# Optimization experiments

Measured on AMD Instinct MI355X. Metric: run time of the kernel, lower is better.

## Reference

```python
import jax, jax.numpy as jnp
import numpy as np

B, C1, C2, D, NH, H, W = 2, 64, 256, 256, 8, 64, 64
HD = D // NH
EPS = 1e-5


def setup_inputs() -> dict:
    key = jax.random.key(0)
    ks = jax.random.split(key, 12)
    s = lambda fan_in: 1.0 / np.sqrt(fan_in)
    return {
        "F_lidar": jax.random.normal(ks[0], (B, C1, H, W), jnp.float32),
        "F_cam": jax.random.normal(ks[1], (B, C2, H, W), jnp.float32),
        "Wq": jax.random.normal(ks[2], (D, C1), jnp.float32) * s(C1),
        "Wk": jax.random.normal(ks[3], (D, C2), jnp.float32) * s(C2),
        "Wv": jax.random.normal(ks[4], (D, C2), jnp.float32) * s(C2),
        "Wo": jax.random.normal(ks[5], (D, D), jnp.float32) * s(D),
        "Wres": jax.random.normal(ks[6], (D, C1), jnp.float32) * s(C1),
        "g1": jnp.ones((D,), jnp.float32),
        "b1": jnp.zeros((D,), jnp.float32),
        "g2": jnp.ones((D,), jnp.float32),
        "b2": jnp.zeros((D,), jnp.float32),
        "W1": jax.random.normal(ks[7], (4 * D, D), jnp.float32) * s(D),
        "bf1": jnp.zeros((4 * D,), jnp.float32),
        "W2": jax.random.normal(ks[8], (D, 4 * D), jnp.float32) * s(4 * D),
        "bf2": jnp.zeros((D,), jnp.float32),
    }


def _layernorm(x, g, b):
    mu = jnp.mean(x, axis=-1, keepdims=True)
    var = jnp.mean(jnp.square(x - mu), axis=-1, keepdims=True)
    return (x - mu) * jax.lax.rsqrt(var + EPS) * g + b


def reference(F_lidar, F_cam, Wq, Wk, Wv, Wo, Wres, g1, b1, g2, b2, W1, bf1, W2, bf2):
    b, _, h, w = F_lidar.shape
    n = h * w
    # channels-last token views: (B, HW, C)
    xl = F_lidar.reshape(b, C1, n).transpose(0, 2, 1)
    xc = F_cam.reshape(b, C2, n).transpose(0, 2, 1)
    # 1x1 conv projections == per-token matmuls
    Q = jnp.einsum('bnc,dc->bnd', xl, Wq).reshape(b, n, NH, HD).transpose(0, 2, 1, 3)
    K = jnp.einsum('bnc,dc->bnd', xc, Wk).reshape(b, n, NH, HD).transpose(0, 2, 1, 3)
    V = jnp.einsum('bnc,dc->bnd', xc, Wv).reshape(b, n, NH, HD).transpose(0, 2, 1, 3)
    scale = HD ** -0.5
    scores = jnp.einsum('bhqd,bhkd->bhqk', Q, K) * scale  # (B,NH,HW,HW)
    attn = jax.nn.softmax(scores, axis=-1)
    out = jnp.einsum('bhqk,bhkd->bhqd', attn, V)
    out = out.transpose(0, 2, 1, 3).reshape(b, n, D)
    out = jnp.einsum('bnd,ed->bne', out, Wo)
    resid = jnp.einsum('bnc,dc->bnd', xl, Wres)
    x = _layernorm(resid + out, g1, b1)
    # FFN (dropout = identity in eval)
    hdn = jax.nn.relu(jnp.einsum('bnd,fd->bnf', x, W1) + bf1)
    ffn = jnp.einsum('bnf,df->bnd', hdn, W2) + bf2
    x = _layernorm(x + ffn, g2, b2)
    return x.transpose(0, 2, 1).reshape(b, D, h, w)
```

## Files before the change

### kernel.cpp

```cpp
#include <hip/hip_runtime.h>
#include <hip/hip_bf16.h>
#include <math.h>

#define NB 2
#define C1 64
#define C2 256
#define DD 256
#define NHH 8
#define HDD 32
#define NN 4096
#define FF 1024
#define MTOT (NB*NN)
#define KVB 128

typedef unsigned short u16;
typedef __attribute__((ext_vector_type(8))) short bf16x8;
typedef __attribute__((ext_vector_type(4))) float f32x4;
typedef __attribute__((ext_vector_type(4))) unsigned short us4;
typedef __attribute__((ext_vector_type(4))) unsigned int u32x4;

__device__ __forceinline__ u16 f2bf(float f) {
    union { float f; unsigned int i; } u; u.f = f;
    unsigned int r = u.i + 0x7FFFu + ((u.i >> 16) & 1u);
    return (u16)(r >> 16);
}

__device__ __forceinline__ unsigned cvt_pk_bf16(float a, float b) {
    unsigned r; asm("v_cvt_pk_bf16_f32 %0, %1, %2" : "=v"(r) : "v"(a), "v"(b)); return r;
}

__device__ __forceinline__ void glds16(const void* g, void* l) {
    __builtin_amdgcn_global_load_lds(
        (__attribute__((address_space(1))) void*)g,
        (__attribute__((address_space(3))) void*)l, 16, 0, 0);
}

__global__ __launch_bounds__(256) void wconv(
    const float* __restrict__ Wq, const float* __restrict__ Wres,
    const float* __restrict__ Wk, const float* __restrict__ Wv,
    const float* __restrict__ Wo, const float* __restrict__ W1,
    const float* __restrict__ W2, u16* __restrict__ d)
{
    int i = blockIdx.x * 256 + threadIdx.x;
    if (i >= 753664) return;
    const float* s; int off;
    if      (i <  16384) { s = Wq;   off = i; }
    else if (i <  32768) { s = Wres; off = i -  16384; }
    else if (i <  98304) { s = Wk;   off = i -  32768; }
    else if (i < 163840) { s = Wv;   off = i -  98304; }
    else if (i < 229376) { s = Wo;   off = i - 163840; }
    else if (i < 491520) { s = W1;   off = i - 229376; }
    else                 { s = W2;   off = i - 491520; }
    d[i] = f2bf(s[off]);
}

__global__ __launch_bounds__(256) void tconv(const float* __restrict__ src,
                                             u16* __restrict__ dst, int C)
{
    __shared__ float tile[64][65];
    const int n0 = blockIdx.x * 64;
    const int c0 = blockIdx.y * 64;
    const int b  = blockIdx.z;
    const int t  = threadIdx.x;
#pragma unroll
    for (int i = 0; i < 4; ++i) {
        int cc = t + i * 256;
        int c = cc >> 4, off = (cc & 15) * 4;
        const float4 v = *(const float4*)&src[((size_t)b*C + c0 + c)*NN + n0 + off];
        tile[c][off+0] = v.x; tile[c][off+1] = v.y;
        tile[c][off+2] = v.z; tile[c][off+3] = v.w;
    }
    __syncthreads();
    const int n = t >> 2, cch = (t & 3) * 16;
    bf16x8 t0, t1;
#pragma unroll
    for (int i = 0; i < 8; ++i) ((u16*)&t0)[i] = f2bf(tile[cch + i][n]);
#pragma unroll
    for (int i = 0; i < 8; ++i) ((u16*)&t1)[i] = f2bf(tile[cch + 8 + i][n]);
    u16* dp = &dst[((size_t)b*NN + n0 + n)*C + c0 + cch];
    *(bf16x8*)&dp[0] = t0;
    *(bf16x8*)&dp[8] = t1;
}

template<int MODE>
__global__ __launch_bounds__(256) void gemm_bt(
    const u16* __restrict__ A, const u16* __restrict__ Bw,
    int M, int N, int K,
    const float* __restrict__ bias, const float* __restrict__ add,
    float* __restrict__ outf, u16* __restrict__ outb, float scale)
{
    __shared__ u16 lA[2][4096];
    __shared__ u16 lB[2][4096];
    const int bm = blockIdx.x * 128;
    const int bn = blockIdx.y * 128;
    const int t = threadIdx.x, lane = t & 63, wid = t >> 6;
    const int wr = (wid >> 1) * 64, wc = (wid & 1) * 64;
    const int lrow = lane & 15, lk = (lane >> 4) * 8;
    const int srow = wid*32 + (lane >> 2);
    const int soff = (lane & 3) * 8;
    const u16* aS = &A[(size_t)(bm + srow)*K + soff];
    const u16* bS = &Bw[(size_t)(bn + srow)*K + soff];
    const int lw = wid * 1024;
    f32x4 acc[4][4] = {};

    glds16(aS,                  &lA[0][lw]);
    glds16(aS + (size_t)16*K,   &lA[0][lw + 512]);
    glds16(bS,                  &lB[0][lw]);
    glds16(bS + (size_t)16*K,   &lB[0][lw + 512]);
    __syncthreads();

    const int nst = K >> 5;
    for (int st = 0; st < nst; ++st) {
        const int cur = st & 1;
        if (st < nst - 1) {
            const int k0 = (st + 1) * 32;
            glds16(aS + k0,                  &lA[cur^1][lw]);
            glds16(aS + (size_t)16*K + k0,   &lA[cur^1][lw + 512]);
            glds16(bS + k0,                  &lB[cur^1][lw]);
            glds16(bS + (size_t)16*K + k0,   &lB[cur^1][lw + 512]);
        }
        bf16x8 af[4], bfr[4];
#pragma unroll
        for (int mf = 0; mf < 4; ++mf)
            af[mf] = *(const bf16x8*)&lA[cur][(wr + mf*16 + lrow)*32 + lk];
#pragma unroll
        for (int nf = 0; nf < 4; ++nf)
            bfr[nf] = *(const bf16x8*)&lB[cur][(wc + nf*16 + lrow)*32 + lk];
#pragma unroll
        for (int mf = 0; mf < 4; ++mf)
#pragma unroll
            for (int nf = 0; nf < 4; ++nf)
                acc[mf][nf] = __builtin_amdgcn_mfma_f32_16x16x32_bf16(af[mf], bfr[nf], acc[mf][nf], 0, 0, 0);
        __syncthreads();
    }
#pragma unroll
    for (int mf = 0; mf < 4; ++mf) {
#pragma unroll
        for (int nf = 0; nf < 4; ++nf) {
#pragma unroll
            for (int j = 0; j < 4; ++j) {
                int row = bm + wr + mf*16 + (lane >> 4)*4 + j;
                int col = bn + wc + nf*16 + lrow;
                float v = acc[mf][nf][j];
                if (MODE == 0) {
                    size_t idx = (size_t)row*N + col;
                    outf[idx] = v + add[idx];
                } else if (MODE == 1) {
                    float r = v + bias[col];
                    outb[(size_t)row*N + col] = f2bf(r > 0.f ? r : 0.f);
                } else if (MODE == 2) {
                    size_t idx = (size_t)row*N + col;
                    outf[idx] = v + bias[col] + add[idx];
                } else if (MODE == 3) {
                    int b = row >> 12, n = row & 4095;
                    if (col < 256) {
                        int h = col >> 5, hd = col & 31;
                        int bh = b*NHH + h;
                        size_t idx = (((size_t)bh*256 + (n >> 4))*64
                                      + (hd >> 3)*16 + (n & 15))*8 + (hd & 7);
                        outb[idx] = f2bf(v);
                    } else {
                        int c = col - 256;
                        int h = c >> 5, hd = c & 31;
                        int hf = hd >> 4, d = hd & 15;
                        int bh = b*NHH + h;
                        int kb = n >> 5, kwb = n & 31;
                        int hp = kwb >> 4, gg = (kwb >> 2) & 3, r = kwb & 3;
                        size_t idx = ((((size_t)bh*128 + kb)*2 + hf)*64 + gg*16 + d)*8
                                   + hp*4 + r;
                        ((u16*)outf)[idx] = f2bf(v);
                    }
                } else {
                    int b = row >> 12, n = row & 4095;
                    if (col < 256) {
                        int h = col >> 5, hd = col & 31;
                        outb[(((size_t)b*NHH + h)*NN + n)*HDD + hd] = f2bf(v * scale);
                    } else {
                        outf[(size_t)row*DD + (col - 256)] = v;
                    }
                }
            }
        }
    }
}

__global__ __launch_bounds__(256) void flash_attn(
    const u16* __restrict__ Qp, const u16* __restrict__ Kperm,
    const u16* __restrict__ Vperm, u16* __restrict__ Op)
{
    __shared__ u16 Kl[2][4096];
    __shared__ u16 Vl[2][4096];
    const int id = blockIdx.x;
    const int sw = (id & 7) * 128 + (id >> 3);
    const int qt = sw & 63;
    const int bh = sw >> 6;
    const size_t base = (size_t)bh * NN * HDD;
    const int t = threadIdx.x, lane = t & 63, w = t >> 6;
    const int q0 = qt * 64;
    const int lrow = lane & 15, g = lane >> 4;

    const bf16x8 qf = *(const bf16x8*)&Qp[base + (size_t)(q0 + w*16 + lrow)*HDD + g*8];

    const u16* kgw = &Kperm[(size_t)bh*131072 + w*1024 + lane*8];
    const u16* vgw = &Vperm[(size_t)bh*131072 + w*1024 + lane*8];
    const int lw = w * 1024;

    u32x4 onesw = {0x3F803F80u, 0x3F803F80u, 0x3F803F80u, 0x3F803F80u};
    const bf16x8 ones = *(bf16x8*)&onesw;

    glds16(kgw,       &Kl[0][lw]);
    glds16(kgw + 512, &Kl[0][lw + 512]);
    glds16(vgw,       &Vl[0][lw]);
    glds16(vgw + 512, &Vl[0][lw + 512]);

    f32x4 o[2] = {};
    f32x4 osum = {};
    __syncthreads();

#define FLASH_STEP(CUR, TT)                                                    \
    {                                                                          \
        if ((TT) < 31) {                                                       \
            const u16* kg = kgw + (size_t)((TT)+1)*4096;                       \
            const u16* vg = vgw + (size_t)((TT)+1)*4096;                       \
            glds16(kg,       &Kl[(CUR)^1][lw]);                                \
            glds16(kg + 512, &Kl[(CUR)^1][lw + 512]);                          \
            glds16(vg,       &Vl[(CUR)^1][lw]);                                \
            glds16(vg + 512, &Vl[(CUR)^1][lw + 512]);                          \
        }                                                                      \
        f32x4 s[8];                                                            \
        __builtin_amdgcn_s_setprio(1);                                         \
        _Pragma("unroll")                                                      \
        for (int nf = 0; nf < 8; ++nf) {                                       \
            bf16x8 kf = *(const bf16x8*)&Kl[(CUR)][nf*512 + lane*8];           \
            f32x4 z = {};                                                      \
            s[nf] = __builtin_amdgcn_mfma_f32_16x16x32_bf16(kf, qf, z, 0, 0, 0); \
        }                                                                      \
        __builtin_amdgcn_s_setprio(0);                                         \
        _Pragma("unroll")                                                      \
        for (int kk = 0; kk < 4; ++kk) {                                       \
            float p0[4], p1[4];                                                \
            _Pragma("unroll")                                                  \
            for (int jj = 0; jj < 4; ++jj) {                                   \
                p0[jj] = __builtin_amdgcn_exp2f(s[2*kk][jj]);                  \
                p1[jj] = __builtin_amdgcn_exp2f(s[2*kk+1][jj]);                 \
            }                                                                  \
            u32x4 paw;                                                         \
            paw[0] = cvt_pk_bf16(p0[0], p0[1]);                                \
            paw[1] = cvt_pk_bf16(p0[2], p0[3]);                                \
            paw[2] = cvt_pk_bf16(p1[0], p1[1]);                                \
            paw[3] = cvt_pk_bf16(p1[2], p1[3]);                                \
            bf16x8 pa = *(bf16x8*)&paw;                                        \
            __builtin_amdgcn_s_setprio(1);                                     \
            _Pragma("unroll")                                                  \
            for (int hf = 0; hf < 2; ++hf) {                                   \
                bf16x8 vf = *(const bf16x8*)&Vl[(CUR)][kk*1024 + hf*512 + lane*8]; \
                o[hf] = __builtin_amdgcn_mfma_f32_16x16x32_bf16(pa, vf, o[hf], 0, 0, 0); \
            }                                                                  \
            osum = __builtin_amdgcn_mfma_f32_16x16x32_bf16(pa, ones, osum, 0, 0, 0); \
            __builtin_amdgcn_s_setprio(0);                                     \
        }                                                                      \
        __syncthreads();                                                       \
    }

    for (int tt = 0; tt < 32; tt += 2) {
        FLASH_STEP(0, tt)
        FLASH_STEP(1, tt + 1)
    }
#undef FLASH_STEP

    const int b = bh >> 3, h = bh & 7;
#pragma unroll
    for (int hf = 0; hf < 2; ++hf)
#pragma unroll
        for (int r = 0; r < 4; ++r) {
            int q = q0 + w*16 + g*4 + r;
            int d = h*HDD + hf*16 + lrow;
            Op[((size_t)b*NN + q)*DD + d] = f2bf(o[hf][r] / osum[r]);
        }
}

__global__ __launch_bounds__(256) void ln_fuse(const float* __restrict__ y,
    const float* __restrict__ g, const float* __restrict__ be,
    float* __restrict__ x, u16* __restrict__ xb)
{
    const int row = blockIdx.x * 4 + (threadIdx.x >> 6);
    const int lane = threadIdx.x & 63;
    const float4 v = *(const float4*)&y[(size_t)row*DD + lane*4];
    float s1 = v.x + v.y + v.z + v.w;
    float s2 = v.x*v.x + v.y*v.y + v.z*v.z + v.w*v.w;
#pragma unroll
    for (int m = 1; m <= 32; m <<= 1) { s1 += __shfl_xor(s1, m); s2 += __shfl_xor(s2, m); }
    float mean = s1 * (1.f/DD);
    float var  = s2 * (1.f/DD) - mean*mean;
    float rstd = rsqrtf(var + 1e-5f);
    const float vv[4] = {v.x, v.y, v.z, v.w};
    float4 xo; us4 xo16;
#pragma unroll
    for (int i = 0; i < 4; ++i) {
        int d = lane*4 + i;
        float r = (vv[i] - mean) * rstd * g[d] + be[d];
        ((float*)&xo)[i] = r;
        xo16[i] = f2bf(r);
    }
    *(float4*)&x[(size_t)row*DD + lane*4] = xo;
    *(us4*)&xb[(size_t)row*DD + lane*4] = xo16;
}

__global__ __launch_bounds__(256) void ln2_transpose(const float* __restrict__ z,
    const float* __restrict__ g, const float* __restrict__ be,
    float* __restrict__ out)
{
    __shared__ float tile[32][257];
    const int n0 = blockIdx.x * 32;
    const int b = blockIdx.y;
    const int t = threadIdx.x, lane = t & 63, w = t >> 6;
    for (int r8 = 0; r8 < 8; ++r8) {
        int r = w*8 + r8;
        const float4 v = *(const float4*)&z[((size_t)b*NN + n0 + r)*DD + lane*4];
        float s1 = v.x + v.y + v.z + v.w;
        float s2 = v.x*v.x + v.y*v.y + v.z*v.z + v.w*v.w;
#pragma unroll
        for (int m = 1; m <= 32; m <<= 1) { s1 += __shfl_xor(s1, m); s2 += __shfl_xor(s2, m); }
        float mean = s1 * (1.f/DD);
        float var  = s2 * (1.f/DD) - mean*mean;
        float rstd = rsqrtf(var + 1e-5f);
        const float vv[4] = {v.x, v.y, v.z, v.w};
#pragma unroll
        for (int i = 0; i < 4; ++i) {
            int d = lane*4 + i;
            tile[r][d] = (vv[i] - mean)*rstd*g[d] + be[d];
        }
    }
    __syncthreads();
    const int n = t & 31, dg = t >> 5;
    for (int dd = 0; dd < 32; ++dd) {
        int d = dd*8 + dg;
        out[((size_t)b*DD + d)*NN + n0 + n] = tile[n][d];
    }
}

extern "C" void kernel_launch(void* const* d_in, const int* in_sizes, int n_in,
                              void* d_out, int out_size, void* d_ws, size_t ws_size,
                              hipStream_t stream)
{
    const float* F_lidar = (const float*)d_in[0];
    const float* F_cam   = (const float*)d_in[1];
    const float* Wq  = (const float*)d_in[2];
    const float* Wk  = (const float*)d_in[3];
    const float* Wv  = (const float*)d_in[4];
    const float* Wo  = (const float*)d_in[5];
    const float* Wrs = (const float*)d_in[6];
    const float* g1  = (const float*)d_in[7];
    const float* b1  = (const float*)d_in[8];
    const float* g2  = (const float*)d_in[9];
    const float* b2  = (const float*)d_in[10];
    const float* W1  = (const float*)d_in[11];
    const float* bf1 = (const float*)d_in[12];
    const float* W2  = (const float*)d_in[13];
    const float* bf2 = (const float*)d_in[14];
    float* out = (float*)d_out;

    char* ws = (char*)d_ws;
    size_t cur = 0;
    auto carve = [&](size_t bytes) {
        size_t o = cur; cur += (bytes + 255) & ~(size_t)255; return (void*)(ws + o);
    };
    u16* wb    = (u16*)carve(753664u * 2);
    u16* xl    = (u16*)carve((size_t)MTOT * C1 * 2);
    u16* xc    = (u16*)carve((size_t)MTOT * C2 * 2);
    u16* Qb    = (u16*)carve((size_t)MTOT * DD * 2);
    u16* Kperm = (u16*)carve((size_t)MTOT * DD * 2);
    u16* Vperm = (u16*)carve((size_t)MTOT * DD * 2);
    float* resid = (float*)carve((size_t)MTOT * DD * 4);
    u16* attn  = (u16*)carve((size_t)MTOT * DD * 2);
    float* y   = (float*)carve((size_t)MTOT * DD * 4);
    float* x   = (float*)carve((size_t)MTOT * DD * 4);
    u16* xb    = (u16*)carve((size_t)MTOT * DD * 2);
    u16* hdn   = (u16*)carve((size_t)MTOT * FF * 2);
    float* zb  = y;

    u16* WqRes = wb;
    u16* WkWv  = wb + 32768;
    u16* Wob   = wb + 163840;
    u16* W1b   = wb + 229376;
    u16* W2b   = wb + 491520;

    wconv<<<2944, 256, 0, stream>>>(Wq, Wrs, Wk, Wv, Wo, W1, W2, wb);
    tconv<<<dim3(64, 1, NB), 256, 0, stream>>>(F_lidar, xl, C1);
    tconv<<<dim3(64, 4, NB), 256, 0, stream>>>(F_cam, xc, C2);

    const float qscale = 1.4426950408889634f / sqrtf((float)HDD);
    gemm_bt<4><<<dim3(64, 4), 256, 0, stream>>>(xl, WqRes, MTOT, 512, C1,
        nullptr, nullptr, resid, Qb, qscale);
    gemm_bt<3><<<dim3(64, 4), 256, 0, stream>>>(xc, WkWv, MTOT, 512, C2,
        nullptr, nullptr, (float*)Vperm, Kperm, 1.f);

    flash_attn<<<1024, 256, 0, stream>>>(Qb, Kperm, Vperm, attn);

    gemm_bt<0><<<dim3(64, 2), 256, 0, stream>>>(attn, Wob, MTOT, DD, DD,
        nullptr, resid, y, nullptr, 1.f);
    ln_fuse<<<2048, 256, 0, stream>>>(y, g1, b1, x, xb);
    gemm_bt<1><<<dim3(64, 8), 256, 0, stream>>>(xb, W1b, MTOT, FF, DD,
        bf1, nullptr, nullptr, hdn, 1.f);
    gemm_bt<2><<<dim3(64, 2), 256, 0, stream>>>(hdn, W2b, MTOT, DD, FF,
        bf2, x, zb, nullptr, 1.f);
    ln2_transpose<<<dim3(128, NB), 256, 0, stream>>>(zb, g2, b2, out);
}
```

Baseline: 141.2 us.

## Merge prep kernels, fuse QKV gemms, use 64-row tiles for N=256 gemms

Combines the weight conversion and both input transposes into one prep kernel with float4-vectorised weight conversion. The two projection GEMMs are merged into a single launch. The Wo and W2 GEMMs get a 64-row tile variant that doubles the block count from 128 to 256, filling more CUs. The goal is fewer launches and better occupancy for the small GEMMs. The cost is more per-block branching and less reuse per block in the smaller tiles.

Result: faster. 123.8 us (-12.3%).

```diff
diff --git a/kernel.cpp b/kernel.cpp
--- a/kernel.cpp
+++ b/kernel.cpp
@@ -35,33 +35,10 @@
         (__attribute__((address_space(3))) void*)l, 16, 0, 0);
 }
 
-__global__ __launch_bounds__(256) void wconv(
-    const float* __restrict__ Wq, const float* __restrict__ Wres,
-    const float* __restrict__ Wk, const float* __restrict__ Wv,
-    const float* __restrict__ Wo, const float* __restrict__ W1,
-    const float* __restrict__ W2, u16* __restrict__ d)
-{
-    int i = blockIdx.x * 256 + threadIdx.x;
-    if (i >= 753664) return;
-    const float* s; int off;
-    if      (i <  16384) { s = Wq;   off = i; }
-    else if (i <  32768) { s = Wres; off = i -  16384; }
-    else if (i <  98304) { s = Wk;   off = i -  32768; }
-    else if (i < 163840) { s = Wv;   off = i -  98304; }
-    else if (i < 229376) { s = Wo;   off = i - 163840; }
-    else if (i < 491520) { s = W1;   off = i - 229376; }
-    else                 { s = W2;   off = i - 491520; }
-    d[i] = f2bf(s[off]);
-}
-
-__global__ __launch_bounds__(256) void tconv(const float* __restrict__ src,
-                                             u16* __restrict__ dst, int C)
-{
-    __shared__ float tile[64][65];
-    const int n0 = blockIdx.x * 64;
-    const int c0 = blockIdx.y * 64;
-    const int b  = blockIdx.z;
-    const int t  = threadIdx.x;
+__device__ __forceinline__ void tconv_body(const float* __restrict__ src,
+    u16* __restrict__ dst, int C, int n0, int c0, int b, int t,
+    float (*tile)[65])
+{
 #pragma unroll
     for (int i = 0; i < 4; ++i) {
         int cc = t + i * 256;
@@ -82,31 +59,64 @@
     *(bf16x8*)&dp[8] = t1;
 }
 
-template<int MODE>
-__global__ __launch_bounds__(256) void gemm_bt(
+__global__ __launch_bounds__(256) void prep(
+    const float* __restrict__ Wq, const float* __restrict__ Wres,
+    const float* __restrict__ Wk, const float* __restrict__ Wv,
+    const float* __restrict__ Wo, const float* __restrict__ W1,
+    const float* __restrict__ W2, u16* __restrict__ d,
+    const float* __restrict__ F_lidar, const float* __restrict__ F_cam,
+    u16* __restrict__ xl, u16* __restrict__ xc)
+{
+    __shared__ float tile[64][65];
+    const int id = blockIdx.x, t = threadIdx.x;
+    if (id < 736) {
+        int i4 = (id * 256 + t) * 4;
+        const float* s; int off;
+        if      (i4 <  16384) { s = Wq;   off = i4; }
+        else if (i4 <  32768) { s = Wres; off = i4 -  16384; }
+        else if (i4 <  98304) { s = Wk;   off = i4 -  32768; }
+        else if (i4 < 163840) { s = Wv;   off = i4 -  98304; }
+        else if (i4 < 229376) { s = Wo;   off = i4 - 163840; }
+        else if (i4 < 491520) { s = W1;   off = i4 - 229376; }
+        else                  { s = W2;   off = i4 - 491520; }
+        const float4 v = *(const float4*)&s[off];
+        us4 o; o[0] = f2bf(v.x); o[1] = f2bf(v.y); o[2] = f2bf(v.z); o[3] = f2bf(v.w);
+        *(us4*)&d[i4] = o;
+    } else if (id < 864) {
+        int l = id - 736;
+        tconv_body(F_lidar, xl, C1, (l & 63)*64, 0, l >> 6, t, tile);
+    } else {
+        int l = id - 864;
+        tconv_body(F_cam, xc, C2, (l & 63)*64, ((l >> 6) & 3)*64, l >> 8, t, tile);
+    }
+}
+
+template<int MODE, int BM>
+__device__ __forceinline__ void gemm_body(
     const u16* __restrict__ A, const u16* __restrict__ Bw,
-    int M, int N, int K,
+    int N, int K,
     const float* __restrict__ bias, const float* __restrict__ add,
-    float* __restrict__ outf, u16* __restrict__ outb, float scale)
-{
-    __shared__ u16 lA[2][4096];
-    __shared__ u16 lB[2][4096];
-    const int bm = blockIdx.x * 128;
-    const int bn = blockIdx.y * 128;
+    float* __restrict__ outf, u16* __restrict__ outb, float scale,
+    int bm, int bn, u16* lA, u16* lB)
+{
+    constexpr int MFR = BM / 32;
+    constexpr int ASZ = BM * 32;
     const int t = threadIdx.x, lane = t & 63, wid = t >> 6;
-    const int wr = (wid >> 1) * 64, wc = (wid & 1) * 64;
+    const int wr = (wid >> 1) * (BM/2), wc = (wid & 1) * 64;
     const int lrow = lane & 15, lk = (lane >> 4) * 8;
-    const int srow = wid*32 + (lane >> 2);
+    const int arow = wid*(BM/4) + (lane >> 2);
+    const int brow = wid*32 + (lane >> 2);
     const int soff = (lane & 3) * 8;
-    const u16* aS = &A[(size_t)(bm + srow)*K + soff];
-    const u16* bS = &Bw[(size_t)(bn + srow)*K + soff];
-    const int lw = wid * 1024;
-    f32x4 acc[4][4] = {};
-
-    glds16(aS,                  &lA[0][lw]);
-    glds16(aS + (size_t)16*K,   &lA[0][lw + 512]);
-    glds16(bS,                  &lB[0][lw]);
-    glds16(bS + (size_t)16*K,   &lB[0][lw + 512]);
+    const u16* aS = &A[(size_t)(bm + arow)*K + soff];
+    const u16* bS = &Bw[(size_t)(bn + brow)*K + soff];
+    const int lwA = wid*(BM/4)*32;
+    const int lwB = wid*1024;
+    f32x4 acc[MFR][4] = {};
+
+    glds16(aS, &lA[lwA]);
+    if (BM == 128) glds16(aS + (size_t)16*K, &lA[lwA + 512]);
+    glds16(bS, &lB[lwB]);
+    glds16(bS + (size_t)16*K, &lB[lwB + 512]);
     __syncthreads();
 
     const int nst = K >> 5;
@@ -114,27 +124,28 @@
         const int cur = st & 1;
         if (st < nst - 1) {
             const int k0 = (st + 1) * 32;
-            glds16(aS + k0,                  &lA[cur^1][lw]);
-            glds16(aS + (size_t)16*K + k0,   &lA[cur^1][lw + 512]);
-            glds16(bS + k0,                  &lB[cur^1][lw]);
-            glds16(bS + (size_t)16*K + k0,   &lB[cur^1][lw + 512]);
+            const int nb = (cur ^ 1);
+            glds16(aS + k0, &lA[nb*ASZ + lwA]);
+            if (BM == 128) glds16(aS + (size_t)16*K + k0, &lA[nb*ASZ + lwA + 512]);
+            glds16(bS + k0, &lB[nb*4096 + lwB]);
+            glds16(bS + (size_t)16*K + k0, &lB[nb*4096 + lwB + 512]);
         }
-        bf16x8 af[4], bfr[4];
-#pragma unroll
-        for (int mf = 0; mf < 4; ++mf)
-            af[mf] = *(const bf16x8*)&lA[cur][(wr + mf*16 + lrow)*32 + lk];
+        bf16x8 af[MFR], bfr[4];
+#pragma unroll
+        for (int mf = 0; mf < MFR; ++mf)
+            af[mf] = *(const bf16x8*)&lA[cur*ASZ + (wr + mf*16 + lrow)*32 + lk];
 #pragma unroll
         for (int nf = 0; nf < 4; ++nf)
-            bfr[nf] = *(const bf16x8*)&lB[cur][(wc + nf*16 + lrow)*32 + lk];
-#pragma unroll
-        for (int mf = 0; mf < 4; ++mf)
+            bfr[nf] = *(const bf16x8*)&lB[cur*4096 + (wc + nf*16 + lrow)*32 + lk];
+#pragma unroll
+        for (int mf = 0; mf < MFR; ++mf)
 #pragma unroll
             for (int nf = 0; nf < 4; ++nf)
                 acc[mf][nf] = __builtin_amdgcn_mfma_f32_16x16x32_bf16(af[mf], bfr[nf], acc[mf][nf], 0, 0, 0);
         __syncthreads();
     }
 #pragma unroll
-    for (int mf = 0; mf < 4; ++mf) {
+    for (int mf = 0; mf < MFR; ++mf) {
 #pragma unroll
         for (int nf = 0; nf < 4; ++nf) {
 #pragma unroll
@@ -162,11 +173,11 @@
                     } else {
                         int c = col - 256;
                         int h = c >> 5, hd = c & 31;
-                        int hf = hd >> 4, d = hd & 15;
+                        int hf = hd >> 4, d2 = hd & 15;
                         int bh = b*NHH + h;
                         int kb = n >> 5, kwb = n & 31;
                         int hp = kwb >> 4, gg = (kwb >> 2) & 3, r = kwb & 3;
-                        size_t idx = ((((size_t)bh*128 + kb)*2 + hf)*64 + gg*16 + d)*8
+                        size_t idx = ((((size_t)bh*128 + kb)*2 + hf)*64 + gg*16 + d2)*8
                                    + hp*4 + r;
                         ((u16*)outf)[idx] = f2bf(v);
                     }
@@ -181,6 +192,37 @@
                 }
             }
         }
+    }
+}
+
+template<int MODE, int BM>
+__global__ __launch_bounds__(256) void gemm_bt(
+    const u16* __restrict__ A, const u16* __restrict__ Bw,
+    int N, int K, const float* __restrict__ bias, const float* __restrict__ add,
+    float* __restrict__ outf, u16* __restrict__ outb, float scale)
+{
+    __shared__ u16 lA[2*BM*32];
+    __shared__ u16 lB[2*4096];
+    gemm_body<MODE, BM>(A, Bw, N, K, bias, add, outf, outb, scale,
+                        blockIdx.x*BM, blockIdx.y*128, lA, lB);
+}
+
+__global__ __launch_bounds__(256) void qkv_gemm(
+    const u16* __restrict__ xl, const u16* __restrict__ xc,
+    const u16* __restrict__ WqRes, const u16* __restrict__ WkWv,
+    float* __restrict__ resid, u16* __restrict__ Qb,
+    u16* __restrict__ Kperm, u16* __restrict__ Vperm, float qscale)
+{
+    __shared__ u16 lA[2*128*32];
+    __shared__ u16 lB[2*4096];
+    int l = blockIdx.x;
+    if (l < 256) {
+        gemm_body<4, 128>(xl, WqRes, 512, 64, nullptr, nullptr, resid, Qb,
+                          qscale, (l & 63)*128, (l >> 6)*128, lA, lB);
+    } else {
+        l -= 256;
+        gemm_body<3, 128>(xc, WkWv, 512, 256, nullptr, nullptr,
+                          (float*)Vperm, Kperm, 1.f, (l & 63)*128, (l >> 6)*128, lA, lB);
     }
 }
 
@@ -385,24 +427,21 @@
     u16* W1b   = wb + 229376;
     u16* W2b   = wb + 491520;
 
-    wconv<<<2944, 256, 0, stream>>>(Wq, Wrs, Wk, Wv, Wo, W1, W2, wb);
-    tconv<<<dim3(64, 1, NB), 256, 0, stream>>>(F_lidar, xl, C1);
-    tconv<<<dim3(64, 4, NB), 256, 0, stream>>>(F_cam, xc, C2);
+    prep<<<1376, 256, 0, stream>>>(Wq, Wrs, Wk, Wv, Wo, W1, W2, wb,
+                                   F_lidar, F_cam, xl, xc);
 
     const float qscale = 1.4426950408889634f / sqrtf((float)HDD);
-    gemm_bt<4><<<dim3(64, 4), 256, 0, stream>>>(xl, WqRes, MTOT, 512, C1,
-        nullptr, nullptr, resid, Qb, qscale);
-    gemm_bt<3><<<dim3(64, 4), 256, 0, stream>>>(xc, WkWv, MTOT, 512, C2,
-        nullptr, nullptr, (float*)Vperm, Kperm, 1.f);
+    qkv_gemm<<<512, 256, 0, stream>>>(xl, xc, WqRes, WkWv,
+                                      resid, Qb, Kperm, Vperm, qscale);
 
     flash_attn<<<1024, 256, 0, stream>>>(Qb, Kperm, Vperm, attn);
 
-    gemm_bt<0><<<dim3(64, 2), 256, 0, stream>>>(attn, Wob, MTOT, DD, DD,
+    gemm_bt<0, 64><<<dim3(128, 2), 256, 0, stream>>>(attn, Wob, DD, DD,
         nullptr, resid, y, nullptr, 1.f);
     ln_fuse<<<2048, 256, 0, stream>>>(y, g1, b1, x, xb);
-    gemm_bt<1><<<dim3(64, 8), 256, 0, stream>>>(xb, W1b, MTOT, FF, DD,
+    gemm_bt<1, 128><<<dim3(64, 8), 256, 0, stream>>>(xb, W1b, FF, DD,
         bf1, nullptr, nullptr, hdn, 1.f);
-    gemm_bt<2><<<dim3(64, 2), 256, 0, stream>>>(hdn, W2b, MTOT, DD, FF,
+    gemm_bt<2, 64><<<dim3(128, 2), 256, 0, stream>>>(hdn, W2b, DD, FF,
         bf2, x, zb, nullptr, 1.f);
     ln2_transpose<<<dim3(128, NB), 256, 0, stream>>>(zb, g2, b2, out);
 }
```
